# Optimization experiments

Hardware: AMD Instinct MI355X
Metric: run time of the kernel (lower is better)

The kernel has to match this reference:

```python
import jax, jax.numpy as jnp
import numpy as np

T, M = 64, 64
ROI, SPA, WORD, I3D = 2048, 4, 300, 1024
H, D = 512, 256  # so_hidden, so_out_dim (= rel_dim)
IN = ROI + SPA + WORD  # 2352


def _w(k, shape):
    return jax.random.normal(k, shape, dtype=jnp.float32) * 0.02


def setup_inputs() -> dict:
    key = jax.random.key(0)
    ks = jax.random.split(key, 32)
    inp = {
        "roi_feats": jax.random.normal(ks[0], (T, M, ROI), dtype=jnp.float32),
        "spatial": jax.random.uniform(ks[1], (T, M, SPA), dtype=jnp.float32),
        "i3d_feats": jax.random.normal(ks[2], (T, I3D), dtype=jnp.float32),
        "subj_emb": jax.random.normal(ks[3], (WORD,), dtype=jnp.float32),
        "obj_emb": jax.random.normal(ks[4], (WORD,), dtype=jnp.float32),
        "pred_emb": jax.random.normal(ks[5], (WORD,), dtype=jnp.float32),
        # subject / object encoders (torch Linear convention: W is (out,in))
        "subj_w1": _w(ks[6], (H, IN)), "subj_b1": _w(ks[7], (H,)),
        "subj_w2": _w(ks[8], (D, H)), "subj_b2": _w(ks[9], (D,)),
        "obj_w1": _w(ks[10], (H, IN)), "obj_b1": _w(ks[11], (H,)),
        "obj_w2": _w(ks[12], (D, H)), "obj_b2": _w(ks[13], (D,)),
        # fuse MLPs (in = 2*D)
        "fuse_s_w1": _w(ks[14], (H, 2 * D)), "fuse_s_b1": _w(ks[15], (H,)),
        "fuse_s_w2": _w(ks[16], (D, H)), "fuse_s_b2": _w(ks[17], (D,)),
        "fuse_o_w1": _w(ks[18], (H, 2 * D)), "fuse_o_b1": _w(ks[19], (H,)),
        "fuse_o_w2": _w(ks[20], (D, H)), "fuse_o_b2": _w(ks[21], (D,)),
        # relation projections + MLP
        "W_rs": _w(ks[22], (D, D)),
        "W_ro": _w(ks[23], (D, D)),
        "rel_w1": _w(ks[24], (H, D + WORD)), "rel_b1": _w(ks[25], (H,)),
        "rel_w2": _w(ks[26], (D, H)), "rel_b2": _w(ks[27], (D,)),
    }
    return inp


def _linear(x, W, b):
    return x @ W.T + b


def _mlp2(x, w1, b1, w2, b2):
    return _linear(jax.nn.relu(_linear(x, w1, b1)), w2, b2)


def reference(roi_feats, spatial, i3d_feats, subj_emb, obj_emb, pred_emb,
              subj_w1, subj_b1, subj_w2, subj_b2,
              obj_w1, obj_b1, obj_w2, obj_b2,
              fuse_s_w1, fuse_s_b1, fuse_s_w2, fuse_s_b2,
              fuse_o_w1, fuse_o_b1, fuse_o_w2, fuse_o_b2,
              W_rs, W_ro, rel_w1, rel_b1, rel_w2, rel_b2):
    Tn, Mn, _ = roi_feats.shape
    se = jnp.broadcast_to(subj_emb, (Tn, Mn, subj_emb.shape[-1]))
    oe = jnp.broadcast_to(obj_emb, (Tn, Mn, obj_emb.shape[-1]))
    # SubjectObjectEncoder: fc2(relu(fc1([roi; spa; word])))
    fs_base = _mlp2(jnp.concatenate([roi_feats, spatial, se], axis=-1),
                    subj_w1, subj_b1, subj_w2, subj_b2)  # (T,M,D)
    fo_base = _mlp2(jnp.concatenate([roi_feats, spatial, oe], axis=-1),
                    obj_w1, obj_b1, obj_w2, obj_b2)
    # use_gsa = use_lla = False -> fuse([base; base])
    fs = _mlp2(jnp.concatenate([fs_base, fs_base], axis=-1),
               fuse_s_w1, fuse_s_b1, fuse_s_w2, fuse_s_b2)
    fo = _mlp2(jnp.concatenate([fo_base, fo_base], axis=-1),
               fuse_o_w1, fuse_o_b1, fuse_o_w2, fuse_o_b2)
    # Eq. 15: pairwise diff + predicate word, then 2-layer MLP
    fs_proj = fs @ W_rs.T
    fo_proj = fo @ W_ro.T
    diff = fs_proj[:, :, None, :] - fo_proj[:, None, :, :]  # (T,M,M,D)
    # rel_fc1([diff; pred]) split into diff part + constant pred part
    Wd, Wp = rel_w1[:, :fs.shape[-1]], rel_w1[:, fs.shape[-1]:]
    h = jax.nn.relu(diff @ Wd.T + (pred_emb @ Wp.T + rel_b1))  # (T,M,M,H)
    return h @ rel_w2.T + rel_b2  # (T,M,M,D)
```

## Files before the change

### kernel.cpp

```cpp
#include <hip/hip_runtime.h>
#include <hip/hip_bf16.h>

typedef __attribute__((ext_vector_type(4))) float f32x4;
typedef __attribute__((ext_vector_type(8))) short s16x8;

__device__ __forceinline__ void async_lds16(const void* g, void* l) {
  __builtin_amdgcn_global_load_lds((const __attribute__((address_space(1))) void*)g,
                                   (__attribute__((address_space(3))) void*)l, 16, 0, 0);
}

__device__ __forceinline__ short f2bf(float x) {
  __hip_bfloat16 h = __float2bfloat16(x);
  short s;
  __builtin_memcpy(&s, &h, 2);
  return s;
}

__device__ __forceinline__ s16x8 pack8(f32x4 a, f32x4 b) {
  s16x8 r;
  r[0] = f2bf(a[0]); r[1] = f2bf(a[1]); r[2] = f2bf(a[2]); r[3] = f2bf(a[3]);
  r[4] = f2bf(b[0]); r[5] = f2bf(b[1]); r[6] = f2bf(b[2]); r[7] = f2bf(b[3]);
  return r;
}

template<bool RELU, bool OUT_BF16, bool HAS_BIAS>
__global__ __launch_bounds__(256) void gemm_bt(
    const __hip_bfloat16* __restrict__ Ag, const __hip_bfloat16* __restrict__ Bg,
    const float* __restrict__ biasg, void* __restrict__ Cg,
    int lda, int ldb, int K, int ldc,
    int strideA, int strideB, int strideBias, long strideC)
{
  __shared__ __align__(16) short As[4096];
  __shared__ __align__(16) short Bs[4096];
  const int tid  = threadIdx.x;
  const int lane = tid & 63;
  const int wid  = tid >> 6;
  const int z    = blockIdx.z;
  const __hip_bfloat16* A = Ag + (long)z * strideA;
  const __hip_bfloat16* B = Bg + (long)z * strideB;
  const float* bias = HAS_BIAS ? (biasg + (long)z * strideBias) : nullptr;
  const int row0 = blockIdx.y * 128;
  const int col0 = blockIdx.x * 128;

  const int srow = wid * 16 + (lane >> 2);
  const int scol = (lane & 3) * 8;

  f32x4 acc[4][4];
#pragma unroll
  for (int i = 0; i < 4; ++i)
#pragma unroll
    for (int j = 0; j < 4; ++j) acc[i][j] = (f32x4)(0.0f);

  const int rw = (wid & 1) * 64;
  const int cw = (wid >> 1) * 64;
  const int lm = lane & 15;
  const int kg = (lane >> 4) * 8;

  for (int ks = 0; ks < K; ks += 32) {
    __syncthreads();
#pragma unroll
    for (int is = 0; is < 2; ++is) {
      async_lds16(A + (long)(row0 + is * 64 + srow) * lda + ks + scol,
                  (char*)As + is * 4096 + wid * 1024);
      async_lds16(B + (long)(col0 + is * 64 + srow) * ldb + ks + scol,
                  (char*)Bs + is * 4096 + wid * 1024);
    }
    __syncthreads();
    s16x8 af[4], bf[4];
#pragma unroll
    for (int mt = 0; mt < 4; ++mt)
      af[mt] = *(const s16x8*)(As + (rw + mt * 16 + lm) * 32 + kg);
#pragma unroll
    for (int nt = 0; nt < 4; ++nt)
      bf[nt] = *(const s16x8*)(Bs + (cw + nt * 16 + lm) * 32 + kg);
#pragma unroll
    for (int mt = 0; mt < 4; ++mt)
#pragma unroll
      for (int nt = 0; nt < 4; ++nt)
        acc[mt][nt] = __builtin_amdgcn_mfma_f32_16x16x32_bf16(af[mt], bf[nt], acc[mt][nt], 0, 0, 0);
  }

  const int lr4 = (lane >> 4) * 4;
#pragma unroll
  for (int mt = 0; mt < 4; ++mt) {
#pragma unroll
    for (int nt = 0; nt < 4; ++nt) {
      const int col = col0 + cw + nt * 16 + lm;
      const float bv = HAS_BIAS ? bias[col] : 0.0f;
#pragma unroll
      for (int r = 0; r < 4; ++r) {
        const int row = row0 + rw + mt * 16 + lr4 + r;
        float v = acc[mt][nt][r] + bv;
        if (RELU) v = fmaxf(v, 0.0f);
        if (OUT_BF16)
          ((__hip_bfloat16*)Cg)[(long)z * strideC + (long)row * ldc + col] = __float2bfloat16(v);
        else
          ((float*)Cg)[(long)z * strideC + (long)row * ldc + col] = v;
      }
    }
  }
}

template<bool RELU, bool OUT_BF16, bool HAS_BIAS>
__global__ __launch_bounds__(256) void gemm_bt64(
    const __hip_bfloat16* __restrict__ Ag, const __hip_bfloat16* __restrict__ Bg,
    const float* __restrict__ biasg, void* __restrict__ Cg,
    int lda, int ldb, int K, int ldc,
    int strideA, int strideB, int strideBias, long strideC)
{
  __shared__ __align__(16) short As[2048];
  __shared__ __align__(16) short Bs[2048];
  const int tid  = threadIdx.x;
  const int lane = tid & 63;
  const int wid  = tid >> 6;
  const int z    = blockIdx.z;
  const __hip_bfloat16* A = Ag + (long)z * strideA;
  const __hip_bfloat16* B = Bg + (long)z * strideB;
  const float* bias = HAS_BIAS ? (biasg + (long)z * strideBias) : nullptr;
  const int row0 = blockIdx.y * 64;
  const int col0 = blockIdx.x * 64;

  const int srow = wid * 16 + (lane >> 2);
  const int scol = (lane & 3) * 8;

  f32x4 acc[2][2];
#pragma unroll
  for (int i = 0; i < 2; ++i)
#pragma unroll
    for (int j = 0; j < 2; ++j) acc[i][j] = (f32x4)(0.0f);

  const int rw = (wid & 1) * 32;
  const int cw = (wid >> 1) * 32;
  const int lm = lane & 15;
  const int kg = (lane >> 4) * 8;

  for (int ks = 0; ks < K; ks += 32) {
    __syncthreads();
    async_lds16(A + (long)(row0 + srow) * lda + ks + scol, (char*)As + wid * 1024);
    async_lds16(B + (long)(col0 + srow) * ldb + ks + scol, (char*)Bs + wid * 1024);
    __syncthreads();
    s16x8 af[2], bf[2];
#pragma unroll
    for (int mt = 0; mt < 2; ++mt)
      af[mt] = *(const s16x8*)(As + (rw + mt * 16 + lm) * 32 + kg);
#pragma unroll
    for (int nt = 0; nt < 2; ++nt)
      bf[nt] = *(const s16x8*)(Bs + (cw + nt * 16 + lm) * 32 + kg);
#pragma unroll
    for (int mt = 0; mt < 2; ++mt)
#pragma unroll
      for (int nt = 0; nt < 2; ++nt)
        acc[mt][nt] = __builtin_amdgcn_mfma_f32_16x16x32_bf16(af[mt], bf[nt], acc[mt][nt], 0, 0, 0);
  }

  const int lr4 = (lane >> 4) * 4;
#pragma unroll
  for (int mt = 0; mt < 2; ++mt) {
#pragma unroll
    for (int nt = 0; nt < 2; ++nt) {
      const int col = col0 + cw + nt * 16 + lm;
      const float bv = HAS_BIAS ? bias[col] : 0.0f;
#pragma unroll
      for (int r = 0; r < 4; ++r) {
        const int row = row0 + rw + mt * 16 + lr4 + r;
        float v = acc[mt][nt][r] + bv;
        if (RELU) v = fmaxf(v, 0.0f);
        if (OUT_BF16)
          ((__hip_bfloat16*)Cg)[(long)z * strideC + (long)row * ldc + col] = __float2bfloat16(v);
        else
          ((float*)Cg)[(long)z * strideC + (long)row * ldc + col] = v;
      }
    }
  }
}

__global__ __launch_bounds__(256) void reduce_relu(
    const float* __restrict__ P, const float* __restrict__ cboth,
    __hip_bfloat16* __restrict__ H1)
{
  const int id = blockIdx.x * 256 + threadIdx.x;
  const int row = id >> 7, c8 = id & 127;
  const f32x4* p0 = (const f32x4*)(P + (long)row * 1024 + c8 * 8);
  const f32x4* p1 = (const f32x4*)(P + 4194304 + (long)row * 1024 + c8 * 8);
  const f32x4* bb = (const f32x4*)(cboth + c8 * 8);
  f32x4 a = p0[0] + p1[0] + bb[0];
  f32x4 b = p0[1] + p1[1] + bb[1];
#pragma unroll
  for (int e = 0; e < 4; ++e) { a[e] = fmaxf(a[e], 0.0f); b[e] = fmaxf(b[e], 0.0f); }
  *(s16x8*)((short*)H1 + (long)row * 1024 + c8 * 8) = pack8(a, b);
}

__global__ __launch_bounds__(256) void rel_final(
    const float* __restrict__ AsBo, const __hip_bfloat16* __restrict__ W2b,
    const float* __restrict__ b2, float* __restrict__ out)
{
  __shared__ __align__(16) short Hs[4096];
  __shared__ __align__(16) short Ws[4096];
  const int tid  = threadIdx.x;
  const int lane = tid & 63;
  const int wid  = tid >> 6;
  const int n0 = blockIdx.x * 128;
  const int i0 = blockIdx.y * 2;
  const int t  = blockIdx.z;

  const float* Ap = AsBo + (long)(t * 64 + i0) * 512;
  const float* Bp = AsBo + 2097152 + (long)t * 64 * 512;

  const int grow = tid >> 1;
  const int gkc  = (tid & 1) * 16;
  const float* arow = Ap + (grow >> 6) * 512 + gkc;
  const float* brow = Bp + (grow & 63) * 512 + gkc;
  short* hdst = Hs + grow * 32 + gkc;

  const int srow = wid * 16 + (lane >> 2);
  const int scol = (lane & 3) * 8;

  f32x4 acc[4][4];
#pragma unroll
  for (int i = 0; i < 4; ++i)
#pragma unroll
    for (int j = 0; j < 4; ++j) acc[i][j] = (f32x4)(0.0f);

  const int rw = (wid & 1) * 64;
  const int cw = (wid >> 1) * 64;
  const int lm = lane & 15;
  const int kg = (lane >> 4) * 8;

  for (int ks = 0; ks < 512; ks += 32) {
    __syncthreads();
#pragma unroll
    for (int is = 0; is < 2; ++is)
      async_lds16(W2b + (long)(n0 + is * 64 + srow) * 512 + ks + scol,
                  (char*)Ws + is * 4096 + wid * 1024);
    f32x4 av[4], bv[4];
#pragma unroll
    for (int q = 0; q < 4; ++q) {
      av[q] = *(const f32x4*)(arow + ks + q * 4);
      bv[q] = *(const f32x4*)(brow + ks + q * 4);
    }
    union { s16x8 v; short s[8]; } p0, p1;
#pragma unroll
    for (int q = 0; q < 2; ++q)
#pragma unroll
      for (int e = 0; e < 4; ++e) {
        p0.s[q * 4 + e] = f2bf(fmaxf(av[q][e] - bv[q][e], 0.0f));
        p1.s[q * 4 + e] = f2bf(fmaxf(av[q + 2][e] - bv[q + 2][e], 0.0f));
      }
    *(s16x8*)hdst = p0.v;
    *(s16x8*)(hdst + 8) = p1.v;
    __syncthreads();
    s16x8 af[4], bf[4];
#pragma unroll
    for (int mt = 0; mt < 4; ++mt)
      af[mt] = *(const s16x8*)(Hs + (rw + mt * 16 + lm) * 32 + kg);
#pragma unroll
    for (int nt = 0; nt < 4; ++nt)
      bf[nt] = *(const s16x8*)(Ws + (cw + nt * 16 + lm) * 32 + kg);
#pragma unroll
    for (int mt = 0; mt < 4; ++mt)
#pragma unroll
      for (int nt = 0; nt < 4; ++nt)
        acc[mt][nt] = __builtin_amdgcn_mfma_f32_16x16x32_bf16(af[mt], bf[nt], acc[mt][nt], 0, 0, 0);
  }

  const int lr4 = (lane >> 4) * 4;
#pragma unroll
  for (int mt = 0; mt < 4; ++mt) {
#pragma unroll
    for (int nt = 0; nt < 4; ++nt) {
      const int col = n0 + cw + nt * 16 + lm;
      const float bv = b2[col];
#pragma unroll
      for (int r = 0; r < 4; ++r) {
        const int prow = rw + mt * 16 + lr4 + r;
        const int il = prow >> 6, j = prow & 63;
        out[(long)((t * 64 + i0 + il) * 64 + j) * 256 + col] = acc[mt][nt][r] + bv;
      }
    }
  }
}

__global__ __launch_bounds__(256) void prep_kernel(
    const float* __restrict__ roi, const float* __restrict__ spatial,
    const float* __restrict__ subj_emb, const float* __restrict__ obj_emb,
    const float* __restrict__ pred_emb,
    const float* __restrict__ subj_w1, const float* __restrict__ subj_b1,
    const float* __restrict__ obj_w1, const float* __restrict__ obj_b1,
    const float* __restrict__ subj_w2, const float* __restrict__ subj_b2,
    const float* __restrict__ obj_w2, const float* __restrict__ obj_b2,
    const float* __restrict__ fs_w1, const float* __restrict__ fs_b1,
    const float* __restrict__ fs_w2, const float* __restrict__ fs_b2,
    const float* __restrict__ fo_w1, const float* __restrict__ fo_b1,
    const float* __restrict__ fo_w2, const float* __restrict__ fo_b2,
    const float* __restrict__ W_rs, const float* __restrict__ W_ro,
    const float* __restrict__ rel_w1, const float* __restrict__ rel_b1,
    const float* __restrict__ rel_w2,
    __hip_bfloat16* __restrict__ XP, __hip_bfloat16* __restrict__ W1P,
    float* __restrict__ cboth,
    __hip_bfloat16* __restrict__ Bcat2, float* __restrict__ bias2,
    __hip_bfloat16* __restrict__ WfCat, float* __restrict__ biasf,
    __hip_bfloat16* __restrict__ W4cat, float* __restrict__ bias4,
    __hip_bfloat16* __restrict__ WcCat, float* __restrict__ crel,
    __hip_bfloat16* __restrict__ W2b)
{
  int id = blockIdx.x * 256 + threadIdx.x;

  if (id < 1081344) {
    int row = id / 264, c8 = id - row * 264;
    s16x8 o;
    if (c8 < 256) {
      const f32x4* src = (const f32x4*)(roi + (long)row * 2048 + c8 * 8);
      o = pack8(src[0], src[1]);
    } else {
      f32x4 a, b;
#pragma unroll
      for (int e = 0; e < 4; ++e) {
        int col = c8 * 8 + e;
        a[e] = (col < 2052) ? spatial[row * 4 + (col - 2048)] : 0.0f;
        int col2 = col + 4;
        b[e] = (col2 < 2052) ? spatial[row * 4 + (col2 - 2048)] : 0.0f;
      }
      o = pack8(a, b);
    }
    *(s16x8*)((short*)XP + (long)id * 8) = o;
    return;
  }
  id -= 1081344;
  if (id < 270336) {
    int row = id / 264, c8 = id - row * 264;
    const float* w = (row < 512) ? (subj_w1 + (long)row * 2352)
                                 : (obj_w1 + (long)(row - 512) * 2352);
    s16x8 o;
    if (c8 < 256) {
      const f32x4* src = (const f32x4*)(w + c8 * 8);
      o = pack8(src[0], src[1]);
    } else {
      f32x4 a, b;
#pragma unroll
      for (int e = 0; e < 4; ++e) {
        int col = c8 * 8 + e;
        a[e] = (col < 2052) ? w[col] : 0.0f;
        int col2 = col + 4;
        b[e] = (col2 < 2052) ? w[col2] : 0.0f;
      }
      o = pack8(a, b);
    }
    *(s16x8*)((short*)W1P + (long)id * 8) = o;
    return;
  }
  id -= 270336;
  if (id < 1024) {
    int h = id;
    const float* w; const float* e; float s;
    if (h < 512) { w = subj_w1 + (long)h * 2352 + 2052; e = subj_emb; s = subj_b1[h]; }
    else { w = obj_w1 + (long)(h - 512) * 2352 + 2052; e = obj_emb; s = obj_b1[h - 512]; }
    for (int k = 0; k < 300; ++k) s += w[k] * e[k];
    cboth[h] = s;
    return;
  }
  id -= 1024;
  if (id < 32768) {
    const float* src = (id < 16384) ? (subj_w2 + id * 8) : (obj_w2 + (id - 16384) * 8);
    const f32x4* s4 = (const f32x4*)src;
    *(s16x8*)((short*)Bcat2 + (long)id * 8) = pack8(s4[0], s4[1]);
    return;
  }
  id -= 32768;
  if (id < 512) { bias2[id] = (id < 256) ? subj_b2[id] : obj_b2[id - 256]; return; }
  id -= 512;
  if (id < 32768) {
    int z = id >> 14, r8 = id & 16383;
    int h = r8 >> 5, d8 = r8 & 31;
    const float* w = (z ? fo_w1 : fs_w1) + h * 512 + d8 * 8;
    const f32x4* lo = (const f32x4*)w;
    const f32x4* hi = (const f32x4*)(w + 256);
    *(s16x8*)((short*)WfCat + (long)id * 8) = pack8(lo[0] + hi[0], lo[1] + hi[1]);
    return;
  }
  id -= 32768;
  if (id < 1024) { biasf[id] = (id < 512) ? fs_b1[id] : fo_b1[id - 512]; return; }
  id -= 1024;
  if (id < 32768) {
    const float* src = (id < 16384) ? (fs_w2 + id * 8) : (fo_w2 + (id - 16384) * 8);
    const f32x4* s4 = (const f32x4*)src;
    *(s16x8*)((short*)W4cat + (long)id * 8) = pack8(s4[0], s4[1]);
    return;
  }
  id -= 32768;
  if (id < 512) { bias4[id] = (id < 256) ? fs_b2[id] : fo_b2[id - 256]; return; }
  id -= 512;
  if (id < 262144) {
    int z = id >> 17, r = id & 131071;
    int h = r >> 8, d = r & 255;
    const float* Wr = z ? W_ro : W_rs;
    const float* wd = rel_w1 + (long)h * 556;
    float s = 0.0f;
    for (int e = 0; e < 256; ++e) s += wd[e] * Wr[e * 256 + d];
    WcCat[id] = __float2bfloat16(s);
    return;
  }
  id -= 262144;
  if (id < 1024) {
    int z = id >> 9, h = id & 511;
    float s = 0.0f;
    if (z == 0) {
      s = rel_b1[h];
      const float* wp = rel_w1 + (long)h * 556 + 256;
      for (int k = 0; k < 300; ++k) s += pred_emb[k] * wp[k];
    }
    crel[id] = s;
    return;
  }
  id -= 1024;
  if (id < 16384) {
    const f32x4* s4 = (const f32x4*)(rel_w2 + id * 8);
    *(s16x8*)((short*)W2b + (long)id * 8) = pack8(s4[0], s4[1]);
  }
}

extern "C" void kernel_launch(void* const* d_in, const int* in_sizes, int n_in,
                              void* d_out, int out_size, void* d_ws, size_t ws_size,
                              hipStream_t stream)
{
  const float* roi       = (const float*)d_in[0];
  const float* spatial   = (const float*)d_in[1];
  const float* subj_emb  = (const float*)d_in[3];
  const float* obj_emb   = (const float*)d_in[4];
  const float* pred_emb  = (const float*)d_in[5];
  const float* subj_w1   = (const float*)d_in[6];
  const float* subj_b1   = (const float*)d_in[7];
  const float* subj_w2   = (const float*)d_in[8];
  const float* subj_b2   = (const float*)d_in[9];
  const float* obj_w1    = (const float*)d_in[10];
  const float* obj_b1    = (const float*)d_in[11];
  const float* obj_w2    = (const float*)d_in[12];
  const float* obj_b2    = (const float*)d_in[13];
  const float* fuse_s_w1 = (const float*)d_in[14];
  const float* fuse_s_b1 = (const float*)d_in[15];
  const float* fuse_s_w2 = (const float*)d_in[16];
  const float* fuse_s_b2 = (const float*)d_in[17];
  const float* fuse_o_w1 = (const float*)d_in[18];
  const float* fuse_o_b1 = (const float*)d_in[19];
  const float* fuse_o_w2 = (const float*)d_in[20];
  const float* fuse_o_b2 = (const float*)d_in[21];
  const float* W_rs      = (const float*)d_in[22];
  const float* W_ro      = (const float*)d_in[23];
  const float* rel_w1    = (const float*)d_in[24];
  const float* rel_b1    = (const float*)d_in[25];
  const float* rel_w2    = (const float*)d_in[26];
  const float* rel_b2    = (const float*)d_in[27];

  char* ws = (char*)d_ws;
  __hip_bfloat16* XP   = (__hip_bfloat16*)(ws);
  float*          AsBo = (float*)(ws);
  __hip_bfloat16* W1P  = (__hip_bfloat16*)(ws + 17301504);
  __hip_bfloat16* H1   = (__hip_bfloat16*)(ws + 21626880);
  __hip_bfloat16* FS   = (__hip_bfloat16*)(ws + 30015488);
  float*          P    = (float*)(ws + 34209792);
  const size_t so = 67764224;
  __hip_bfloat16* Bcat2 = (__hip_bfloat16*)(ws + so);
  float*          bias2 = (float*)(ws + so + 524288);
  __hip_bfloat16* WfCat = (__hip_bfloat16*)(ws + so + 526336);
  float*          biasf = (float*)(ws + so + 1050624);
  __hip_bfloat16* W4cat = (__hip_bfloat16*)(ws + so + 1054720);
  float*          bias4 = (float*)(ws + so + 1579008);
  __hip_bfloat16* WcCat = (__hip_bfloat16*)(ws + so + 1581056);
  float*          crel  = (float*)(ws + so + 2105344);
  __hip_bfloat16* W2b   = (__hip_bfloat16*)(ws + so + 2109440);
  float*          cboth = (float*)(ws + so + 2371584);

  prep_kernel<<<6768, 256, 0, stream>>>(
      roi, spatial, subj_emb, obj_emb, pred_emb,
      subj_w1, subj_b1, obj_w1, obj_b1, subj_w2, subj_b2, obj_w2, obj_b2,
      fuse_s_w1, fuse_s_b1, fuse_s_w2, fuse_s_b2,
      fuse_o_w1, fuse_o_b1, fuse_o_w2, fuse_o_b2,
      W_rs, W_ro, rel_w1, rel_b1, rel_w2,
      XP, W1P, cboth, Bcat2, bias2, WfCat, biasf, W4cat, bias4, WcCat, crel, W2b);

  gemm_bt<false, false, false><<<dim3(8, 32, 2), 256, 0, stream>>>(
      XP, W1P, cboth, P, 2112, 2112, 1056, 1024, 1056, 1056, 0, 4194304L);
  reduce_relu<<<2048, 256, 0, stream>>>(P, cboth, H1);
  gemm_bt64<false, true, true><<<dim3(4, 64, 2), 256, 0, stream>>>(
      H1, Bcat2, bias2, FS, 1024, 512, 512, 512, 512, 131072, 256, 256);
  gemm_bt64<true, true, true><<<dim3(8, 64, 2), 256, 0, stream>>>(
      FS, WfCat, biasf, H1, 512, 256, 256, 1024, 256, 131072, 512, 512);
  gemm_bt64<false, true, true><<<dim3(4, 64, 2), 256, 0, stream>>>(
      H1, W4cat, bias4, FS, 1024, 512, 512, 512, 512, 131072, 256, 256);
  gemm_bt64<false, false, true><<<dim3(8, 64, 2), 256, 0, stream>>>(
      FS, WcCat, crel, AsBo, 512, 256, 256, 512, 256, 131072, 512, 2097152L);
  rel_final<<<dim3(2, 32, 64), 256, 0, stream>>>(AsBo, W2b, rel_b2, (float*)d_out);
}
```

Baseline: 573.8 us.

## Widen rel_final tile to all 256 columns and swizzle the H LDS tile

```diff
diff --git a/kernel.cpp b/kernel.cpp
--- a/kernel.cpp
+++ b/kernel.cpp
@@ -195,13 +195,12 @@
     const float* __restrict__ b2, float* __restrict__ out)
 {
   __shared__ __align__(16) short Hs[4096];
-  __shared__ __align__(16) short Ws[4096];
+  __shared__ __align__(16) short Ws[8192];
   const int tid  = threadIdx.x;
   const int lane = tid & 63;
   const int wid  = tid >> 6;
-  const int n0 = blockIdx.x * 128;
-  const int i0 = blockIdx.y * 2;
-  const int t  = blockIdx.z;
+  const int i0 = blockIdx.x * 2;
+  const int t  = blockIdx.y;
 
   const float* Ap = AsBo + (long)(t * 64 + i0) * 512;
   const float* Bp = AsBo + 2097152 + (long)t * 64 * 512;
@@ -210,28 +209,29 @@
   const int gkc  = (tid & 1) * 16;
   const float* arow = Ap + (grow >> 6) * 512 + gkc;
   const float* brow = Bp + (grow & 63) * 512 + gkc;
-  short* hdst = Hs + grow * 32 + gkc;
-
-  const int srow = wid * 16 + (lane >> 2);
-  const int scol = (lane & 3) * 8;
-
-  f32x4 acc[4][4];
+  const int hbyte = (grow * 64 + (tid & 1) * 32) ^ ((grow & 7) << 4);
+
+  const int wsrow = lane >> 2;
+  const int wscol = (lane & 3) * 8;
+
+  f32x4 acc[4][8];
 #pragma unroll
   for (int i = 0; i < 4; ++i)
 #pragma unroll
-    for (int j = 0; j < 4; ++j) acc[i][j] = (f32x4)(0.0f);
+    for (int j = 0; j < 8; ++j) acc[i][j] = (f32x4)(0.0f);
 
   const int rw = (wid & 1) * 64;
-  const int cw = (wid >> 1) * 64;
+  const int cw = (wid >> 1) * 128;
   const int lm = lane & 15;
   const int kg = (lane >> 4) * 8;
+  const int hrbase = (lm * 64 + kg * 2) ^ ((lm & 7) << 4);
 
   for (int ks = 0; ks < 512; ks += 32) {
     __syncthreads();
 #pragma unroll
-    for (int is = 0; is < 2; ++is)
-      async_lds16(W2b + (long)(n0 + is * 64 + srow) * 512 + ks + scol,
-                  (char*)Ws + is * 4096 + wid * 1024);
+    for (int q = 0; q < 4; ++q)
+      async_lds16(W2b + (long)(wid * 64 + q * 16 + wsrow) * 512 + ks + wscol,
+                  (char*)Ws + wid * 4096 + q * 1024);
     f32x4 av[4], bv[4];
 #pragma unroll
     for (int q = 0; q < 4; ++q) {
@@ -246,35 +246,36 @@
         p0.s[q * 4 + e] = f2bf(fmaxf(av[q][e] - bv[q][e], 0.0f));
         p1.s[q * 4 + e] = f2bf(fmaxf(av[q + 2][e] - bv[q + 2][e], 0.0f));
       }
-    *(s16x8*)hdst = p0.v;
-    *(s16x8*)(hdst + 8) = p1.v;
-    __syncthreads();
-    s16x8 af[4], bf[4];
+    *(s16x8*)((char*)Hs + hbyte) = p0.v;
+    *(s16x8*)((char*)Hs + (hbyte ^ 16)) = p1.v;
+    __syncthreads();
+    s16x8 af[4], bf[8];
 #pragma unroll
     for (int mt = 0; mt < 4; ++mt)
-      af[mt] = *(const s16x8*)(Hs + (rw + mt * 16 + lm) * 32 + kg);
-#pragma unroll
-    for (int nt = 0; nt < 4; ++nt)
+      af[mt] = *(const s16x8*)((char*)Hs + (rw + mt * 16) * 64 + hrbase);
+#pragma unroll
+    for (int nt = 0; nt < 8; ++nt)
       bf[nt] = *(const s16x8*)(Ws + (cw + nt * 16 + lm) * 32 + kg);
 #pragma unroll
     for (int mt = 0; mt < 4; ++mt)
 #pragma unroll
-      for (int nt = 0; nt < 4; ++nt)
+      for (int nt = 0; nt < 8; ++nt)
         acc[mt][nt] = __builtin_amdgcn_mfma_f32_16x16x32_bf16(af[mt], bf[nt], acc[mt][nt], 0, 0, 0);
   }
 
   const int lr4 = (lane >> 4) * 4;
+  const long obase = (long)(t * 64 + i0) * 64 * 256;
 #pragma unroll
   for (int mt = 0; mt < 4; ++mt) {
 #pragma unroll
-    for (int nt = 0; nt < 4; ++nt) {
-      const int col = n0 + cw + nt * 16 + lm;
-      const float bv = b2[col];
+    for (int nt = 0; nt < 8; ++nt) {
+      const int col = cw + nt * 16 + lm;
+      const float bvv = b2[col];
 #pragma unroll
       for (int r = 0; r < 4; ++r) {
         const int prow = rw + mt * 16 + lr4 + r;
         const int il = prow >> 6, j = prow & 63;
-        out[(long)((t * 64 + i0 + il) * 64 + j) * 256 + col] = acc[mt][nt][r] + bv;
+        out[obase + (long)(il * 64 + j) * 256 + col] = acc[mt][nt][r] + bvv;
       }
     }
   }
@@ -488,5 +489,5 @@
       H1, W4cat, bias4, FS, 1024, 512, 512, 512, 512, 131072, 256, 256);
   gemm_bt64<false, false, true><<<dim3(8, 64, 2), 256, 0, stream>>>(
       FS, WcCat, crel, AsBo, 512, 256, 256, 512, 256, 131072, 512, 2097152L);
-  rel_final<<<dim3(2, 32, 64), 256, 0, stream>>>(AsBo, W2b, rel_b2, (float*)d_out);
-}
+  rel_final<<<dim3(32, 64), 256, 0, stream>>>(AsBo, W2b, rel_b2, (float*)d_out);
+}
```

After: 630.7 us. 9.9% more time.

## Restructure rel_final: per-(t,i) block, register-built A fragments, double-buffered swizzled W2

Applied to the files above, without the earlier changes.

```diff
diff --git a/kernel.cpp b/kernel.cpp
--- a/kernel.cpp
+++ b/kernel.cpp
@@ -190,91 +190,124 @@
   *(s16x8*)((short*)H1 + (long)row * 1024 + c8 * 8) = pack8(a, b);
 }
 
-__global__ __launch_bounds__(256) void rel_final(
+__global__ __launch_bounds__(256, 2) void rel_final(
     const float* __restrict__ AsBo, const __hip_bfloat16* __restrict__ W2b,
     const float* __restrict__ b2, float* __restrict__ out)
 {
-  __shared__ __align__(16) short Hs[4096];
-  __shared__ __align__(16) short Ws[4096];
+  __shared__ __align__(16) short Ws[2][16384];
   const int tid  = threadIdx.x;
   const int lane = tid & 63;
   const int wid  = tid >> 6;
-  const int n0 = blockIdx.x * 128;
-  const int i0 = blockIdx.y * 2;
-  const int t  = blockIdx.z;
-
-  const float* Ap = AsBo + (long)(t * 64 + i0) * 512;
+  const int bid = (int)blockIdx.x;
+  const int swz = (bid & 7) * 512 + (bid >> 3);
+  const int t = swz >> 6;
+  const int i = swz & 63;
+
+  const float* Ap = AsBo + (long)(t * 64 + i) * 512;
   const float* Bp = AsBo + 2097152 + (long)t * 64 * 512;
 
-  const int grow = tid >> 1;
-  const int gkc  = (tid & 1) * 16;
-  const float* arow = Ap + (grow >> 6) * 512 + gkc;
-  const float* brow = Bp + (grow & 63) * 512 + gkc;
-  short* hdst = Hs + grow * 32 + gkc;
-
-  const int srow = wid * 16 + (lane >> 2);
-  const int scol = (lane & 3) * 8;
+  const int lm   = lane & 15;
+  const int kgrp = lane >> 4;
+
+  const char* w2src = (const char*)W2b
+      + (long)(wid * 64 + (lane >> 3)) * 1024
+      + ((((lane & 7) ^ (lane >> 3))) << 4);
+
+  const int off0 = (kgrp * 16) ^ ((lm & 7) << 4);
 
   f32x4 acc[4][4];
 #pragma unroll
-  for (int i = 0; i < 4; ++i)
-#pragma unroll
-    for (int j = 0; j < 4; ++j) acc[i][j] = (f32x4)(0.0f);
-
-  const int rw = (wid & 1) * 64;
-  const int cw = (wid >> 1) * 64;
-  const int lm = lane & 15;
-  const int kg = (lane >> 4) * 8;
-
-  for (int ks = 0; ks < 512; ks += 32) {
+  for (int a = 0; a < 4; ++a)
+#pragma unroll
+    for (int b = 0; b < 4; ++b) acc[a][b] = (f32x4)(0.0f);
+
+  f32x4 apf[2][2];
+  f32x4 bpf[4][2][2];
+#pragma unroll
+  for (int kf = 0; kf < 2; ++kf) {
+    apf[kf][0] = *(const f32x4*)(Ap + kf * 32 + kgrp * 8);
+    apf[kf][1] = *(const f32x4*)(Ap + kf * 32 + kgrp * 8 + 4);
+  }
+#pragma unroll
+  for (int mt = 0; mt < 4; ++mt)
+#pragma unroll
+    for (int kf = 0; kf < 2; ++kf) {
+      const float* br = Bp + (mt * 16 + lm) * 512 + kf * 32 + kgrp * 8;
+      bpf[mt][kf][0] = *(const f32x4*)(br);
+      bpf[mt][kf][1] = *(const f32x4*)(br + 4);
+    }
+#pragma unroll
+  for (int q = 0; q < 8; ++q)
+    async_lds16(w2src + q * 8192, (char*)Ws[0] + wid * 8192 + q * 1024);
+  __syncthreads();
+
+#pragma unroll
+  for (int ch = 0; ch < 8; ++ch) {
+    const int cur = ch & 1;
+    s16x8 bf[4][2];
+#pragma unroll
+    for (int nt = 0; nt < 4; ++nt)
+#pragma unroll
+      for (int kf = 0; kf < 2; ++kf)
+        bf[nt][kf] = *(const s16x8*)((char*)Ws[cur] + wid * 8192 + nt * 2048
+                                     + lm * 128 + (off0 ^ (kf * 64)));
+    s16x8 af[4][2];
+#pragma unroll
+    for (int mt = 0; mt < 4; ++mt)
+#pragma unroll
+      for (int kf = 0; kf < 2; ++kf) {
+        f32x4 d0, d1;
+#pragma unroll
+        for (int e = 0; e < 4; ++e) {
+          d0[e] = fmaxf(apf[kf][0][e] - bpf[mt][kf][0][e], 0.0f);
+          d1[e] = fmaxf(apf[kf][1][e] - bpf[mt][kf][1][e], 0.0f);
+        }
+        af[mt][kf] = pack8(d0, d1);
+      }
+    if (ch < 7) {
+      const int ko = (ch + 1) * 64;
+#pragma unroll
+      for (int kf = 0; kf < 2; ++kf) {
+        apf[kf][0] = *(const f32x4*)(Ap + ko + kf * 32 + kgrp * 8);
+        apf[kf][1] = *(const f32x4*)(Ap + ko + kf * 32 + kgrp * 8 + 4);
+      }
+#pragma unroll
+      for (int mt = 0; mt < 4; ++mt)
+#pragma unroll
+        for (int kf = 0; kf < 2; ++kf) {
+          const float* br = Bp + (mt * 16 + lm) * 512 + ko + kf * 32 + kgrp * 8;
+          bpf[mt][kf][0] = *(const f32x4*)(br);
+          bpf[mt][kf][1] = *(const f32x4*)(br + 4);
+        }
+#pragma unroll
+      for (int q = 0; q < 8; ++q)
+        async_lds16(w2src + (ch + 1) * 128 + q * 8192,
+                    (char*)Ws[cur ^ 1] + wid * 8192 + q * 1024);
+    }
+    __builtin_amdgcn_s_setprio(1);
+#pragma unroll
+    for (int mt = 0; mt < 4; ++mt)
+#pragma unroll
+      for (int nt = 0; nt < 4; ++nt)
+#pragma unroll
+        for (int kf = 0; kf < 2; ++kf)
+          acc[mt][nt] = __builtin_amdgcn_mfma_f32_16x16x32_bf16(
+              af[mt][kf], bf[nt][kf], acc[mt][nt], 0, 0, 0);
+    __builtin_amdgcn_s_setprio(0);
     __syncthreads();
-#pragma unroll
-    for (int is = 0; is < 2; ++is)
-      async_lds16(W2b + (long)(n0 + is * 64 + srow) * 512 + ks + scol,
-                  (char*)Ws + is * 4096 + wid * 1024);
-    f32x4 av[4], bv[4];
-#pragma unroll
-    for (int q = 0; q < 4; ++q) {
-      av[q] = *(const f32x4*)(arow + ks + q * 4);
-      bv[q] = *(const f32x4*)(brow + ks + q * 4);
-    }
-    union { s16x8 v; short s[8]; } p0, p1;
-#pragma unroll
-    for (int q = 0; q < 2; ++q)
-#pragma unroll
-      for (int e = 0; e < 4; ++e) {
-        p0.s[q * 4 + e] = f2bf(fmaxf(av[q][e] - bv[q][e], 0.0f));
-        p1.s[q * 4 + e] = f2bf(fmaxf(av[q + 2][e] - bv[q + 2][e], 0.0f));
-      }
-    *(s16x8*)hdst = p0.v;
-    *(s16x8*)(hdst + 8) = p1.v;
-    __syncthreads();
-    s16x8 af[4], bf[4];
-#pragma unroll
-    for (int mt = 0; mt < 4; ++mt)
-      af[mt] = *(const s16x8*)(Hs + (rw + mt * 16 + lm) * 32 + kg);
-#pragma unroll
-    for (int nt = 0; nt < 4; ++nt)
-      bf[nt] = *(const s16x8*)(Ws + (cw + nt * 16 + lm) * 32 + kg);
-#pragma unroll
-    for (int mt = 0; mt < 4; ++mt)
-#pragma unroll
-      for (int nt = 0; nt < 4; ++nt)
-        acc[mt][nt] = __builtin_amdgcn_mfma_f32_16x16x32_bf16(af[mt], bf[nt], acc[mt][nt], 0, 0, 0);
-  }
-
-  const int lr4 = (lane >> 4) * 4;
+  }
+
+  const long obase = (long)(t * 64 + i) * 16384;
 #pragma unroll
   for (int mt = 0; mt < 4; ++mt) {
 #pragma unroll
     for (int nt = 0; nt < 4; ++nt) {
-      const int col = n0 + cw + nt * 16 + lm;
-      const float bv = b2[col];
+      const int col = wid * 64 + nt * 16 + lm;
+      const float bvv = b2[col];
 #pragma unroll
       for (int r = 0; r < 4; ++r) {
-        const int prow = rw + mt * 16 + lr4 + r;
-        const int il = prow >> 6, j = prow & 63;
-        out[(long)((t * 64 + i0 + il) * 64 + j) * 256 + col] = acc[mt][nt][r] + bv;
+        const int j = mt * 16 + kgrp * 4 + r;
+        out[obase + j * 256 + col] = acc[mt][nt][r] + bvv;
       }
     }
   }
@@ -488,5 +521,5 @@
       H1, W4cat, bias4, FS, 1024, 512, 512, 512, 512, 131072, 256, 256);
   gemm_bt64<false, false, true><<<dim3(8, 64, 2), 256, 0, stream>>>(
       FS, WcCat, crel, AsBo, 512, 256, 256, 512, 256, 131072, 512, 2097152L);
-  rel_final<<<dim3(2, 32, 64), 256, 0, stream>>>(AsBo, W2b, rel_b2, (float*)d_out);
-}
+  rel_final<<<4096, 256, 0, stream>>>(AsBo, W2b, rel_b2, (float*)d_out);
+}
```

New measurement: 731.1 us. 1.27x slower.
